# Kernel tuning notes

Hardware: AMD Instinct MI355X
Metric: run time of the kernel (lower is better)

Reference implementation:

```python
import jax, jax.numpy as jnp
import numpy as np

N_NODES = 100000
N_EDGES = 600000
IN_C, HID_C, OUT_C = 128, 128, 64


def gcn_conv(x, W, b, src, dst, n_nodes):
    """PyG GCNConv: out = D^{-1/2} (A + I) D^{-1/2} X W + b (symmetric norm, self-loops)."""
    h = x @ W  # [N, C_out] transform first (as PyG does)
    # add self loops
    loop = jnp.arange(n_nodes, dtype=src.dtype)
    s = jnp.concatenate([src, loop])
    d = jnp.concatenate([dst, loop])
    # degree over targets (edge weight = 1)
    deg = jax.ops.segment_sum(jnp.ones_like(d, dtype=h.dtype), d, num_segments=n_nodes)
    dinv = jnp.where(deg > 0, jax.lax.rsqrt(deg), 0.0)
    norm = dinv[s] * dinv[d]  # [E+N]
    msg = h[s] * norm[:, None]  # gather + scale
    out = jax.ops.segment_sum(msg, d, num_segments=n_nodes)  # scatter-add
    return out + b


def setup_inputs() -> dict:
    key = jax.random.key(0)
    k1, k2, k3, k4, k5 = jax.random.split(key, 5)
    x = jax.random.normal(k1, (N_NODES, IN_C), dtype=jnp.float32)
    src = jax.random.randint(k2, (N_EDGES,), 0, N_NODES, dtype=jnp.int32)
    dst = jax.random.randint(k3, (N_EDGES,), 0, N_NODES, dtype=jnp.int32)
    # Glorot-style init for conv weights, zero bias (PyG defaults)
    W1 = jax.random.normal(k4, (IN_C, HID_C), dtype=jnp.float32) * (1.0 / np.sqrt(IN_C))
    W2 = jax.random.normal(k5, (HID_C, OUT_C), dtype=jnp.float32) * (1.0 / np.sqrt(HID_C))
    b1 = jnp.zeros((HID_C,), dtype=jnp.float32)
    b2 = jnp.zeros((OUT_C,), dtype=jnp.float32)
    return {"x": x, "W1": W1, "b1": b1, "W2": W2, "b2": b2, "src": src, "dst": dst}


def reference(x, W1, b1, W2, b2, src, dst):
    h = gcn_conv(x, W1, b1, src, dst, N_NODES)
    h = jax.nn.relu(h)
    out = gcn_conv(h, W2, b2, src, dst, N_NODES)
    return out
```

## Files before the change

### kernel.cpp

```cpp
#include <hip/hip_runtime.h>
#include <math.h>


typedef __bf16 bf16x8 __attribute__((ext_vector_type(8)));
typedef float f32x4 __attribute__((ext_vector_type(4)));

union ABu {
  unsigned short u16[8];
  uint4 u4;
  bf16x8 v;
};

__device__ inline unsigned short f2bf(float f) {
  unsigned u = __float_as_uint(f);
  return (unsigned short)((u + 0x7fffu + ((u >> 16) & 1u)) >> 16);
}

__device__ inline void unpack8(uint4 v, float* f) {
  f[0] = __uint_as_float(v.x << 16);
  f[1] = __uint_as_float(v.x & 0xffff0000u);
  f[2] = __uint_as_float(v.y << 16);
  f[3] = __uint_as_float(v.y & 0xffff0000u);
  f[4] = __uint_as_float(v.z << 16);
  f[5] = __uint_as_float(v.z & 0xffff0000u);
  f[6] = __uint_as_float(v.w << 16);
  f[7] = __uint_as_float(v.w & 0xffff0000u);
}

__device__ inline uint4 pack8(const float* a) {
  uint4 o;
  o.x = (unsigned)f2bf(a[0]) | ((unsigned)f2bf(a[1]) << 16);
  o.y = (unsigned)f2bf(a[2]) | ((unsigned)f2bf(a[3]) << 16);
  o.z = (unsigned)f2bf(a[4]) | ((unsigned)f2bf(a[5]) << 16);
  o.w = (unsigned)f2bf(a[6]) | ((unsigned)f2bf(a[7]) << 16);
  return o;
}

constexpr int SCAN_CHUNK = 1024;

__global__ void k_zero_i32(int* __restrict__ p, int n) {
  int i = blockIdx.x * blockDim.x + threadIdx.x;
  if (i < n) p[i] = 0;
}

__global__ __launch_bounds__(256) void k_count_convW(const int* __restrict__ dst,
                                                     int* __restrict__ counts,
                                                     const float* __restrict__ W1,
                                                     const float* __restrict__ W2,
                                                     unsigned short* __restrict__ Wb1,
                                                     unsigned short* __restrict__ Wb2,
                                                     int E) {
  constexpr int CONV_BLOCKS = (128 * 128 + 128 * 64) / 256;
  if (blockIdx.x < CONV_BLOCKS) {
    int idx = blockIdx.x * 256 + threadIdx.x;
    if (idx < 128 * 128) {
      int k = idx >> 7, n = idx & 127;
      Wb1[(((k >> 3) << 7) + n) * 8 + (k & 7)] = f2bf(W1[idx]);
    } else {
      int j = idx - 128 * 128;
      int k = j >> 6, n = j & 63;
      Wb2[(((k >> 3) << 6) + n) * 8 + (k & 7)] = f2bf(W2[j]);
    }
    return;
  }
  int e = (blockIdx.x - CONV_BLOCKS) * 256 + threadIdx.x;
  if (e < E) atomicAdd(&counts[dst[e]], 1);
}

__global__ __launch_bounds__(256) void k_scan1(const int* __restrict__ counts,
                                               int* __restrict__ offsets,
                                               int* __restrict__ aux, int n) {
  __shared__ int tsum[256];
  int tid = threadIdx.x;
  int base = blockIdx.x * SCAN_CHUNK + tid * 4;
  int v0 = (base + 0 < n) ? counts[base + 0] : 0;
  int v1 = (base + 1 < n) ? counts[base + 1] : 0;
  int v2 = (base + 2 < n) ? counts[base + 2] : 0;
  int v3 = (base + 3 < n) ? counts[base + 3] : 0;
  int s = v0 + v1 + v2 + v3;
  tsum[tid] = s;
  __syncthreads();
  for (int off = 1; off < 256; off <<= 1) {
    int t = (tid >= off) ? tsum[tid - off] : 0;
    __syncthreads();
    tsum[tid] += t;
    __syncthreads();
  }
  int excl = tsum[tid] - s;
  if (base + 0 < n) offsets[base + 0] = excl;
  if (base + 1 < n) offsets[base + 1] = excl + v0;
  if (base + 2 < n) offsets[base + 2] = excl + v0 + v1;
  if (base + 3 < n) offsets[base + 3] = excl + v0 + v1 + v2;
  if (tid == 255) aux[blockIdx.x] = tsum[255];
}

__global__ __launch_bounds__(256) void k_scan3_dinv(int* __restrict__ offsets,
                                                    const int* __restrict__ aux,
                                                    int* __restrict__ cursor,
                                                    const int* __restrict__ counts,
                                                    float* __restrict__ dinv,
                                                    int n, int E, int G) {
  __shared__ int saux[256];
  int tid = threadIdx.x;
  int v = (tid < G) ? aux[tid] : 0;
  saux[tid] = v;
  __syncthreads();
  for (int off = 1; off < 256; off <<= 1) {
    int t = (tid >= off) ? saux[tid - off] : 0;
    __syncthreads();
    saux[tid] += t;
    __syncthreads();
  }
  int excl = saux[tid] - v;
  __syncthreads();
  saux[tid] = excl;
  __syncthreads();

  int i = blockIdx.x * 256 + tid;
  if (i < n) {
    int o = offsets[i] + saux[i >> 10];
    offsets[i] = o;
    cursor[i] = o;
    dinv[i] = rsqrtf((float)(counts[i] + 1));
  }
  if (i == 0) offsets[n] = E;
}

__global__ __launch_bounds__(256) void k_fill_gemm1(const int* __restrict__ src,
                                                    const int* __restrict__ dst,
                                                    int* __restrict__ cursor,
                                                    int* __restrict__ esrc, int E, int FB,
                                                    const float* __restrict__ X,
                                                    const unsigned short* __restrict__ Wb,
                                                    const float* __restrict__ dinv,
                                                    unsigned short* __restrict__ Cb,
                                                    int M) {
  if (blockIdx.x < FB) {
    int e = blockIdx.x * 256 + threadIdx.x;
    if (e < E) {
      int s = src[e];
      int d = dst[e];
      int pos = atomicAdd(&cursor[d], 1);
      esrc[pos] = s;
    }
    return;
  }

  constexpr int K = 128, N = 128, NT = N / 16, KS = K / 32;
  const int bid = blockIdx.x - FB;
  const int tid = threadIdx.x;
  const int wave = tid >> 6;
  const int lane = tid & 63;
  const int q = lane >> 4;
  const int l15 = lane & 15;
  const int row0 = bid * 64 + wave * 16;
  const int rowA = row0 + l15;

  f32x4 zero = {0.0f, 0.0f, 0.0f, 0.0f};
  f32x4 acc[NT];
#pragma unroll
  for (int t = 0; t < NT; ++t) acc[t] = zero;

#pragma unroll
  for (int kk = 0; kk < KS; ++kk) {
    ABu a;
    float4 f0 = make_float4(0.f, 0.f, 0.f, 0.f);
    float4 f1 = make_float4(0.f, 0.f, 0.f, 0.f);
    if (rowA < M) {
      const float4* ap = (const float4*)(X + (size_t)rowA * K + kk * 32 + q * 8);
      f0 = ap[0];
      f1 = ap[1];
    }
    a.u16[0] = f2bf(f0.x); a.u16[1] = f2bf(f0.y);
    a.u16[2] = f2bf(f0.z); a.u16[3] = f2bf(f0.w);
    a.u16[4] = f2bf(f1.x); a.u16[5] = f2bf(f1.y);
    a.u16[6] = f2bf(f1.z); a.u16[7] = f2bf(f1.w);
#pragma unroll
    for (int nt = 0; nt < NT; ++nt) {
      ABu b;
      b.u4 = *(const uint4*)(Wb + ((size_t)(kk * 4 + q) * N + nt * 16 + l15) * 8);
      acc[nt] = __builtin_amdgcn_mfma_f32_16x16x32_bf16(a.v, b.v, acc[nt], 0, 0, 0);
    }
  }

#pragma unroll
  for (int v = 0; v < 4; ++v) {
    int row = row0 + q * 4 + v;
    if (row < M) {
      float di = dinv[row];
#pragma unroll
      for (int nt = 0; nt < NT; ++nt)
        Cb[(size_t)row * N + nt * 16 + l15] = f2bf(acc[nt][v] * di);
    }
  }
}

__global__ __launch_bounds__(256) void k_aggemm(const unsigned short* __restrict__ h1s,
                                                const float* __restrict__ dinv,
                                                const float* __restrict__ b1,
                                                const int* __restrict__ offsets,
                                                const int* __restrict__ esrc,
                                                const unsigned short* __restrict__ Wb2,
                                                unsigned short* __restrict__ h2s,
                                                int n) {
  constexpr int LDA = 136;
  __shared__ unsigned short As[16 * LDA];
  __shared__ float sdinv[16];
  const int tid = threadIdx.x;

  {
    const int nl = tid >> 4;
    const int q = tid & 15;
    const int node = blockIdx.x * 16 + nl;
    float acc[8];
    if (node < n) {
      const uint4* h4 = (const uint4*)h1s;
      float di = dinv[node];
      if (q == 0) sdinv[nl] = di;
      unpack8(h4[(size_t)node * 16 + q], acc);
      int e0 = offsets[node];
      int e1 = offsets[node + 1];
      int e = e0;
      for (; e + 3 < e1; e += 4) {
        int s0 = esrc[e + 0];
        int s1 = esrc[e + 1];
        int s2 = esrc[e + 2];
        int s3 = esrc[e + 3];
        uint4 r0 = h4[(size_t)s0 * 16 + q];
        uint4 r1 = h4[(size_t)s1 * 16 + q];
        uint4 r2 = h4[(size_t)s2 * 16 + q];
        uint4 r3 = h4[(size_t)s3 * 16 + q];
        float g0[8], g1[8], g2[8], g3[8];
        unpack8(r0, g0);
        unpack8(r1, g1);
        unpack8(r2, g2);
        unpack8(r3, g3);
#pragma unroll
        for (int i = 0; i < 8; ++i) acc[i] += (g0[i] + g1[i]) + (g2[i] + g3[i]);
      }
      for (; e < e1; ++e) {
        float gv[8];
        unpack8(h4[(size_t)esrc[e] * 16 + q], gv);
#pragma unroll
        for (int i = 0; i < 8; ++i) acc[i] += gv[i];
      }
      const float4* b14 = (const float4*)b1;
      float4 ba = b14[q * 2], bb = b14[q * 2 + 1];
      float bias[8] = {ba.x, ba.y, ba.z, ba.w, bb.x, bb.y, bb.z, bb.w};
#pragma unroll
      for (int i = 0; i < 8; ++i) acc[i] = fmaxf(fmaf(acc[i], di, bias[i]), 0.f);
    } else {
      if (q == 0) sdinv[nl] = 0.f;
#pragma unroll
      for (int i = 0; i < 8; ++i) acc[i] = 0.f;
    }
    *(uint4*)&As[nl * LDA + q * 8] = pack8(acc);
  }
  __syncthreads();

  {
    const int wave = tid >> 6;
    const int lane = tid & 63;
    const int q = lane >> 4;
    const int l15 = lane & 15;
    f32x4 acc = {0.0f, 0.0f, 0.0f, 0.0f};
#pragma unroll
    for (int kk = 0; kk < 4; ++kk) {
      ABu a, b;
      a.u4 = *(const uint4*)&As[l15 * LDA + kk * 32 + q * 8];
      b.u4 = *(const uint4*)(Wb2 + ((size_t)(kk * 4 + q) * 64 + wave * 16 + l15) * 8);
      acc = __builtin_amdgcn_mfma_f32_16x16x32_bf16(a.v, b.v, acc, 0, 0, 0);
    }
#pragma unroll
    for (int v = 0; v < 4; ++v) {
      int rl = q * 4 + v;
      int row = blockIdx.x * 16 + rl;
      if (row < n) h2s[(size_t)row * 64 + wave * 16 + l15] = f2bf(acc[v] * sdinv[rl]);
    }
  }
}

__global__ __launch_bounds__(256) void k_agg2(const unsigned short* __restrict__ h2s,
                                              const float* __restrict__ dinv,
                                              const float* __restrict__ b2,
                                              const int* __restrict__ offsets,
                                              const int* __restrict__ esrc,
                                              float* __restrict__ out, int n) {
  constexpr int CQ = 8;
  const int tid = threadIdx.x;
  const int node = blockIdx.x * 32 + tid / CQ;
  const int q = tid % CQ;
  if (node >= n) return;

  const uint4* h4 = (const uint4*)h2s;
  float di = dinv[node];
  float acc[8];
  unpack8(h4[(size_t)node * CQ + q], acc);

  int e0 = offsets[node];
  int e1 = offsets[node + 1];
  int e = e0;
  for (; e + 3 < e1; e += 4) {
    int s0 = esrc[e + 0];
    int s1 = esrc[e + 1];
    int s2 = esrc[e + 2];
    int s3 = esrc[e + 3];
    uint4 r0 = h4[(size_t)s0 * CQ + q];
    uint4 r1 = h4[(size_t)s1 * CQ + q];
    uint4 r2 = h4[(size_t)s2 * CQ + q];
    uint4 r3 = h4[(size_t)s3 * CQ + q];
    float g0[8], g1[8], g2[8], g3[8];
    unpack8(r0, g0);
    unpack8(r1, g1);
    unpack8(r2, g2);
    unpack8(r3, g3);
#pragma unroll
    for (int i = 0; i < 8; ++i) acc[i] += (g0[i] + g1[i]) + (g2[i] + g3[i]);
  }
  for (; e < e1; ++e) {
    float gv[8];
    unpack8(h4[(size_t)esrc[e] * CQ + q], gv);
#pragma unroll
    for (int i = 0; i < 8; ++i) acc[i] += gv[i];
  }

  const float4* b24 = (const float4*)b2;
  float4 ba = b24[q * 2], bb = b24[q * 2 + 1];
  float bias[8] = {ba.x, ba.y, ba.z, ba.w, bb.x, bb.y, bb.z, bb.w};
  float4 o0, o1;
  o0.x = fmaf(acc[0], di, bias[0]);
  o0.y = fmaf(acc[1], di, bias[1]);
  o0.z = fmaf(acc[2], di, bias[2]);
  o0.w = fmaf(acc[3], di, bias[3]);
  o1.x = fmaf(acc[4], di, bias[4]);
  o1.y = fmaf(acc[5], di, bias[5]);
  o1.z = fmaf(acc[6], di, bias[6]);
  o1.w = fmaf(acc[7], di, bias[7]);
  ((float4*)out)[(size_t)node * 16 + q * 2 + 0] = o0;
  ((float4*)out)[(size_t)node * 16 + q * 2 + 1] = o1;
}


extern "C" void kernel_launch(void* const* d_in, const int* in_sizes, int n_in,
                              void* d_out, int out_size, void* d_ws, size_t ws_size,
                              hipStream_t stream) {
  const float* x  = (const float*)d_in[0];
  const float* W1 = (const float*)d_in[1];
  const float* b1 = (const float*)d_in[2];
  const float* W2 = (const float*)d_in[3];
  const float* b2 = (const float*)d_in[4];
  const int* src  = (const int*)d_in[5];
  const int* dst  = (const int*)d_in[6];
  float* out = (float*)d_out;

  constexpr int IN_C = 128, HID_C = 128, OUT_C = 64;
  const int N = in_sizes[0] / IN_C;
  const int E = in_sizes[5];

  char* p = (char*)d_ws;
  auto alloc = [&](size_t bytes) {
    char* r = p;
    p += (bytes + 255) & ~(size_t)255;
    return r;
  };
  float* dinv    = (float*)alloc((size_t)N * 4);
  int*   offsets = (int*)alloc((size_t)(N + 1) * 4);
  int*   counts  = (int*)alloc((size_t)N * 4);
  int*   cursor  = (int*)alloc((size_t)N * 4);
  int*   aux     = (int*)alloc(1024);
  int*   esrc    = (int*)alloc((size_t)E * 4);
  unsigned short* Wb1 = (unsigned short*)alloc((size_t)IN_C * HID_C * 2);
  unsigned short* Wb2 = (unsigned short*)alloc((size_t)HID_C * OUT_C * 2);
  unsigned short* h1s = (unsigned short*)alloc((size_t)N * HID_C * 2);
  unsigned short* h2s = (unsigned short*)alloc((size_t)N * OUT_C * 2);

  const int T = 256;
  const int G = (N + SCAN_CHUNK - 1) / SCAN_CHUNK;
  const int FB = (E + T - 1) / T;
  const int GB = (N + 63) / 64;
  constexpr int CONV_BLOCKS = (128 * 128 + 128 * 64) / 256;

  k_zero_i32<<<(N + T - 1) / T, T, 0, stream>>>(counts, N);
  k_count_convW<<<CONV_BLOCKS + FB, T, 0, stream>>>(dst, counts, W1, W2, Wb1, Wb2, E);
  k_scan1<<<G, T, 0, stream>>>(counts, offsets, aux, N);
  k_scan3_dinv<<<(N + T - 1) / T, T, 0, stream>>>(offsets, aux, cursor, counts, dinv, N, E, G);
  k_fill_gemm1<<<FB + GB, T, 0, stream>>>(src, dst, cursor, esrc, E, FB, x, Wb1, dinv, h1s, N);
  k_aggemm<<<(N + 15) / 16, T, 0, stream>>>(h1s, dinv, b1, offsets, esrc, Wb2, h2s, N);
  k_agg2<<<(N + 31) / 32, T, 0, stream>>>(h2s, dinv, b2, offsets, esrc, out, N);
}
```

Before: 230.0 us.

## Split GEMM1 across count and fill kernels, move source scaling into gather

Result: slower. 246.0 us (+7.0%).

```diff
diff --git a/kernel.cpp b/kernel.cpp
--- a/kernel.cpp
+++ b/kernel.cpp
@@ -38,33 +38,93 @@
 
 constexpr int SCAN_CHUNK = 1024;
 
-__global__ void k_zero_i32(int* __restrict__ p, int n) {
-  int i = blockIdx.x * blockDim.x + threadIdx.x;
-  if (i < n) p[i] = 0;
-}
-
-__global__ __launch_bounds__(256) void k_count_convW(const int* __restrict__ dst,
-                                                     int* __restrict__ counts,
-                                                     const float* __restrict__ W1,
-                                                     const float* __restrict__ W2,
-                                                     unsigned short* __restrict__ Wb1,
-                                                     unsigned short* __restrict__ Wb2,
-                                                     int E) {
+__device__ inline void gemm1_tile(const float* __restrict__ X,
+                                  const unsigned short* __restrict__ Wb,
+                                  unsigned short* __restrict__ Cb, int M,
+                                  int row0w, int tid) {
+  constexpr int K = 128, N = 128, NT = N / 16, KS = K / 32;
+  const int wave = tid >> 6;
+  const int lane = tid & 63;
+  const int q = lane >> 4;
+  const int l15 = lane & 15;
+  const int row0 = row0w + wave * 16;
+  const int rowA = row0 + l15;
+
+  f32x4 zero = {0.0f, 0.0f, 0.0f, 0.0f};
+  f32x4 acc[NT];
+#pragma unroll
+  for (int t = 0; t < NT; ++t) acc[t] = zero;
+
+#pragma unroll
+  for (int kk = 0; kk < KS; ++kk) {
+    ABu a;
+    float4 f0 = make_float4(0.f, 0.f, 0.f, 0.f);
+    float4 f1 = make_float4(0.f, 0.f, 0.f, 0.f);
+    if (rowA < M) {
+      const float4* ap = (const float4*)(X + (size_t)rowA * K + kk * 32 + q * 8);
+      f0 = ap[0];
+      f1 = ap[1];
+    }
+    a.u16[0] = f2bf(f0.x); a.u16[1] = f2bf(f0.y);
+    a.u16[2] = f2bf(f0.z); a.u16[3] = f2bf(f0.w);
+    a.u16[4] = f2bf(f1.x); a.u16[5] = f2bf(f1.y);
+    a.u16[6] = f2bf(f1.z); a.u16[7] = f2bf(f1.w);
+#pragma unroll
+    for (int nt = 0; nt < NT; ++nt) {
+      ABu b;
+      b.u4 = *(const uint4*)(Wb + ((size_t)(kk * 4 + q) * N + nt * 16 + l15) * 8);
+      acc[nt] = __builtin_amdgcn_mfma_f32_16x16x32_bf16(a.v, b.v, acc[nt], 0, 0, 0);
+    }
+  }
+
+#pragma unroll
+  for (int v = 0; v < 4; ++v) {
+    int row = row0 + q * 4 + v;
+    if (row < M) {
+#pragma unroll
+      for (int nt = 0; nt < NT; ++nt)
+        Cb[(size_t)row * N + nt * 16 + l15] = f2bf(acc[nt][v]);
+    }
+  }
+}
+
+__global__ __launch_bounds__(256) void k_pre(const float* __restrict__ W1,
+                                             const float* __restrict__ W2,
+                                             unsigned short* __restrict__ Wb1,
+                                             unsigned short* __restrict__ Wb2,
+                                             int* __restrict__ counts, int n) {
   constexpr int CONV_BLOCKS = (128 * 128 + 128 * 64) / 256;
   if (blockIdx.x < CONV_BLOCKS) {
     int idx = blockIdx.x * 256 + threadIdx.x;
     if (idx < 128 * 128) {
-      int k = idx >> 7, n = idx & 127;
-      Wb1[(((k >> 3) << 7) + n) * 8 + (k & 7)] = f2bf(W1[idx]);
+      int k = idx >> 7, c = idx & 127;
+      Wb1[(((k >> 3) << 7) + c) * 8 + (k & 7)] = f2bf(W1[idx]);
     } else {
       int j = idx - 128 * 128;
-      int k = j >> 6, n = j & 63;
-      Wb2[(((k >> 3) << 6) + n) * 8 + (k & 7)] = f2bf(W2[j]);
+      int k = j >> 6, c = j & 63;
+      Wb2[(((k >> 3) << 6) + c) * 8 + (k & 7)] = f2bf(W2[j]);
     }
     return;
   }
-  int e = (blockIdx.x - CONV_BLOCKS) * 256 + threadIdx.x;
-  if (e < E) atomicAdd(&counts[dst[e]], 1);
+  int i = (blockIdx.x - CONV_BLOCKS) * 256 + threadIdx.x;
+  if (i < n) counts[i] = 0;
+}
+
+__global__ __launch_bounds__(256) void k_count_gemm1a(const int* __restrict__ dst,
+                                                      int* __restrict__ counts, int E,
+                                                      const float* __restrict__ X,
+                                                      const unsigned short* __restrict__ Wb,
+                                                      unsigned short* __restrict__ Cb,
+                                                      int M, int CGRP) {
+  const int g = blockIdx.x >> 2;
+  const int r = blockIdx.x & 3;
+  if (r < 3) {
+    int cid = g * 3 + r;
+    int e = cid * 256 + threadIdx.x;
+    if (e < E) atomicAdd(&counts[dst[e]], 1);
+    return;
+  }
+  gemm1_tile(X, Wb, Cb, M, g * 64, threadIdx.x);
 }
 
 __global__ __launch_bounds__(256) void k_scan1(const int* __restrict__ counts,
@@ -126,17 +186,19 @@
   if (i == 0) offsets[n] = E;
 }
 
-__global__ __launch_bounds__(256) void k_fill_gemm1(const int* __restrict__ src,
-                                                    const int* __restrict__ dst,
-                                                    int* __restrict__ cursor,
-                                                    int* __restrict__ esrc, int E, int FB,
-                                                    const float* __restrict__ X,
-                                                    const unsigned short* __restrict__ Wb,
-                                                    const float* __restrict__ dinv,
-                                                    unsigned short* __restrict__ Cb,
-                                                    int M) {
-  if (blockIdx.x < FB) {
-    int e = blockIdx.x * 256 + threadIdx.x;
+__global__ __launch_bounds__(256) void k_fill_gemm1b(const int* __restrict__ src,
+                                                     const int* __restrict__ dst,
+                                                     int* __restrict__ cursor,
+                                                     int* __restrict__ esrc, int E,
+                                                     const float* __restrict__ X,
+                                                     const unsigned short* __restrict__ Wb,
+                                                     unsigned short* __restrict__ Cb,
+                                                     int M, int ROW0) {
+  const int g = blockIdx.x >> 2;
+  const int r = blockIdx.x & 3;
+  if (r < 3) {
+    int fid = g * 3 + r;
+    int e = fid * 256 + threadIdx.x;
     if (e < E) {
       int s = src[e];
       int d = dst[e];
@@ -145,54 +207,7 @@
     }
     return;
   }
-
-  constexpr int K = 128, N = 128, NT = N / 16, KS = K / 32;
-  const int bid = blockIdx.x - FB;
-  const int tid = threadIdx.x;
-  const int wave = tid >> 6;
-  const int lane = tid & 63;
-  const int q = lane >> 4;
-  const int l15 = lane & 15;
-  const int row0 = bid * 64 + wave * 16;
-  const int rowA = row0 + l15;
-
-  f32x4 zero = {0.0f, 0.0f, 0.0f, 0.0f};
-  f32x4 acc[NT];
-#pragma unroll
-  for (int t = 0; t < NT; ++t) acc[t] = zero;
-
-#pragma unroll
-  for (int kk = 0; kk < KS; ++kk) {
-    ABu a;
-    float4 f0 = make_float4(0.f, 0.f, 0.f, 0.f);
-    float4 f1 = make_float4(0.f, 0.f, 0.f, 0.f);
-    if (rowA < M) {
-      const float4* ap = (const float4*)(X + (size_t)rowA * K + kk * 32 + q * 8);
-      f0 = ap[0];
-      f1 = ap[1];
-    }
-    a.u16[0] = f2bf(f0.x); a.u16[1] = f2bf(f0.y);
-    a.u16[2] = f2bf(f0.z); a.u16[3] = f2bf(f0.w);
-    a.u16[4] = f2bf(f1.x); a.u16[5] = f2bf(f1.y);
-    a.u16[6] = f2bf(f1.z); a.u16[7] = f2bf(f1.w);
-#pragma unroll
-    for (int nt = 0; nt < NT; ++nt) {
-      ABu b;
-      b.u4 = *(const uint4*)(Wb + ((size_t)(kk * 4 + q) * N + nt * 16 + l15) * 8);
-      acc[nt] = __builtin_amdgcn_mfma_f32_16x16x32_bf16(a.v, b.v, acc[nt], 0, 0, 0);
-    }
-  }
-
-#pragma unroll
-  for (int v = 0; v < 4; ++v) {
-    int row = row0 + q * 4 + v;
-    if (row < M) {
-      float di = dinv[row];
-#pragma unroll
-      for (int nt = 0; nt < NT; ++nt)
-        Cb[(size_t)row * N + nt * 16 + l15] = f2bf(acc[nt][v] * di);
-    }
-  }
+  gemm1_tile(X, Wb, Cb, M, ROW0 + g * 64, threadIdx.x);
 }
 
 __global__ __launch_bounds__(256) void k_aggemm(const unsigned short* __restrict__ h1s,
@@ -217,32 +232,34 @@
       const uint4* h4 = (const uint4*)h1s;
       float di = dinv[node];
       if (q == 0) sdinv[nl] = di;
-      unpack8(h4[(size_t)node * 16 + q], acc);
+      float hs[8];
+      unpack8(h4[(size_t)node * 16 + q], hs);
+#pragma unroll
+      for (int i = 0; i < 8; ++i) acc[i] = hs[i] * di;
       int e0 = offsets[node];
       int e1 = offsets[node + 1];
-      int e = e0;
-      for (; e + 3 < e1; e += 4) {
-        int s0 = esrc[e + 0];
-        int s1 = esrc[e + 1];
-        int s2 = esrc[e + 2];
-        int s3 = esrc[e + 3];
-        uint4 r0 = h4[(size_t)s0 * 16 + q];
-        uint4 r1 = h4[(size_t)s1 * 16 + q];
-        uint4 r2 = h4[(size_t)s2 * 16 + q];
-        uint4 r3 = h4[(size_t)s3 * 16 + q];
-        float g0[8], g1[8], g2[8], g3[8];
-        unpack8(r0, g0);
-        unpack8(r1, g1);
-        unpack8(r2, g2);
-        unpack8(r3, g3);
-#pragma unroll
-        for (int i = 0; i < 8; ++i) acc[i] += (g0[i] + g1[i]) + (g2[i] + g3[i]);
-      }
-      for (; e < e1; ++e) {
-        float gv[8];
-        unpack8(h4[(size_t)esrc[e] * 16 + q], gv);
-#pragma unroll
-        for (int i = 0; i < 8; ++i) acc[i] += gv[i];
+      for (int e = e0; e < e1; e += 8) {
+        int idx[8];
+#pragma unroll
+        for (int i = 0; i < 8; ++i) {
+          int ee = e + i < e1 ? e + i : e1 - 1;
+          idx[i] = esrc[ee];
+        }
+        uint4 rr[8];
+        float dv[8];
+#pragma unroll
+        for (int i = 0; i < 8; ++i) {
+          rr[i] = h4[(size_t)idx[i] * 16 + q];
+          dv[i] = dinv[idx[i]];
+        }
+#pragma unroll
+        for (int i = 0; i < 8; ++i) {
+          float w = (e + i < e1) ? dv[i] : 0.f;
+          float g[8];
+          unpack8(rr[i], g);
+#pragma unroll
+          for (int j = 0; j < 8; ++j) acc[j] = fmaf(g[j], w, acc[j]);
+        }
       }
       const float4* b14 = (const float4*)b1;
       float4 ba = b14[q * 2], bb = b14[q * 2 + 1];
@@ -299,29 +316,24 @@
 
   int e0 = offsets[node];
   int e1 = offsets[node + 1];
-  int e = e0;
-  for (; e + 3 < e1; e += 4) {
-    int s0 = esrc[e + 0];
-    int s1 = esrc[e + 1];
-    int s2 = esrc[e + 2];
-    int s3 = esrc[e + 3];
-    uint4 r0 = h4[(size_t)s0 * CQ + q];
-    uint4 r1 = h4[(size_t)s1 * CQ + q];
-    uint4 r2 = h4[(size_t)s2 * CQ + q];
-    uint4 r3 = h4[(size_t)s3 * CQ + q];
-    float g0[8], g1[8], g2[8], g3[8];
-    unpack8(r0, g0);
-    unpack8(r1, g1);
-    unpack8(r2, g2);
-    unpack8(r3, g3);
-#pragma unroll
-    for (int i = 0; i < 8; ++i) acc[i] += (g0[i] + g1[i]) + (g2[i] + g3[i]);
-  }
-  for (; e < e1; ++e) {
-    float gv[8];
-    unpack8(h4[(size_t)esrc[e] * CQ + q], gv);
-#pragma unroll
-    for (int i = 0; i < 8; ++i) acc[i] += gv[i];
+  for (int e = e0; e < e1; e += 8) {
+    int idx[8];
+#pragma unroll
+    for (int i = 0; i < 8; ++i) {
+      int ee = e + i < e1 ? e + i : e1 - 1;
+      idx[i] = esrc[ee];
+    }
+    uint4 rr[8];
+#pragma unroll
+    for (int i = 0; i < 8; ++i) rr[i] = h4[(size_t)idx[i] * CQ + q];
+#pragma unroll
+    for (int i = 0; i < 8; ++i) {
+      float w = (e + i < e1) ? 1.f : 0.f;
+      float g[8];
+      unpack8(rr[i], g);
+#pragma unroll
+      for (int j = 0; j < 8; ++j) acc[j] = fmaf(g[j], w, acc[j]);
+    }
   }
 
   const float4* b24 = (const float4*)b2;
@@ -376,15 +388,26 @@
 
   const int T = 256;
   const int G = (N + SCAN_CHUNK - 1) / SCAN_CHUNK;
-  const int FB = (E + T - 1) / T;
+  const int EB = (E + T - 1) / T;
   const int GB = (N + 63) / 64;
   constexpr int CONV_BLOCKS = (128 * 128 + 128 * 64) / 256;
 
-  k_zero_i32<<<(N + T - 1) / T, T, 0, stream>>>(counts, N);
-  k_count_convW<<<CONV_BLOCKS + FB, T, 0, stream>>>(dst, counts, W1, W2, Wb1, Wb2, E);
+  const int EGRP = (EB + 2) / 3;
+  const int GA = GB < EGRP ? GB : EGRP;
+  const int GBb = GB - GA;
+  const int ROW0 = GA * 64;
+
+  k_pre<<<CONV_BLOCKS + (N + T - 1) / T, T, 0, stream>>>(W1, W2, Wb1, Wb2, counts, N);
+  {
+    int grp = EGRP > GA ? EGRP : GA;
+    k_count_gemm1a<<<4 * grp, T, 0, stream>>>(dst, counts, E, x, Wb1, h1s, N, GA);
+  }
   k_scan1<<<G, T, 0, stream>>>(counts, offsets, aux, N);
   k_scan3_dinv<<<(N + T - 1) / T, T, 0, stream>>>(offsets, aux, cursor, counts, dinv, N, E, G);
-  k_fill_gemm1<<<FB + GB, T, 0, stream>>>(src, dst, cursor, esrc, E, FB, x, Wb1, dinv, h1s, N);
+  {
+    int grp = EGRP > GBb ? EGRP : GBb;
+    k_fill_gemm1b<<<4 * grp, T, 0, stream>>>(src, dst, cursor, esrc, E, x, Wb1, h1s, N, ROW0);
+  }
   k_aggemm<<<(N + 15) / 16, T, 0, stream>>>(h1s, dinv, b1, offsets, esrc, Wb2, h2s, N);
   k_agg2<<<(N + 31) / 32, T, 0, stream>>>(h2s, dinv, b2, offsets, esrc, out, N);
 }
```
